# Kernel optimization log

Hardware: AMD Instinct MI355X
Metric: run time of the kernel (lower is better)

## Reference

```python
import jax, jax.numpy as jnp
import numpy as np
from jax.ops import segment_sum

N_NODES = 50000
N_EDGES = 800000
IN_DIM, HID_DIM, OUT_DIM = 128, 256, 128


def _glorot(key, shape):
    lim = np.sqrt(6.0 / (shape[0] + shape[1]))
    return jax.random.uniform(key, shape, jnp.float32, -lim, lim)


def setup_inputs() -> dict:
    key = jax.random.key(0)
    ks = jax.random.split(key, 4)
    x = jax.random.normal(ks[0], (N_NODES, IN_DIM), jnp.float32)
    edge_index = jax.random.randint(ks[1], (2, N_EDGES), 0, N_NODES, jnp.int64)
    W1 = _glorot(ks[2], (IN_DIM, HID_DIM))
    b1 = jnp.zeros((HID_DIM,), jnp.float32)
    W2 = _glorot(ks[3], (HID_DIM, OUT_DIM))
    b2 = jnp.zeros((OUT_DIM,), jnp.float32)
    return {"x": x, "edge_index": edge_index, "W1": W1, "b1": b1, "W2": W2, "b2": b2}


def gcn_conv(x, W, b, src, dst, n_nodes):
    # PyG GCNConv: x' = D^{-1/2} (A + I) D^{-1/2} (x W) + b
    h = x @ W  # [N, F_out]
    deg = segment_sum(jnp.ones_like(src, dtype=h.dtype), dst, num_segments=n_nodes) + 1.0  # +1 self loop
    dinv = jax.lax.rsqrt(deg)  # [N]
    norm = dinv[src] * dinv[dst]  # per-edge norm [E]
    msg = h[src] * norm[:, None]  # [E, F_out]
    agg = segment_sum(msg, dst, num_segments=n_nodes)
    agg = agg + h * (dinv * dinv)[:, None]  # self-loop term: norm_ii = dinv_i^2
    return agg + b


def reference(x, edge_index, W1, b1, W2, b2):
    src, dst = edge_index[0], edge_index[1]
    h = gcn_conv(x, W1, b1, src, dst, N_NODES)
    h = jax.nn.relu(h)
    out = gcn_conv(h, W2, b2, src, dst, N_NODES)
    return out
```

## Files before the change

kernel.cpp:

```cpp
#include <hip/hip_runtime.h>

#define N_NODES 50000
#define N_EDGES 800000
#define IN_DIM  128
#define HID_DIM 256
#define OUT_DIM 128
#define BUCKET_CAP 64
#define NCOARSE 391
#define BINSZ 128
#define CHUNK 4000
#define NBLK1 200
#define SEGCAP 32
#define HLD 264
#define GROWS 64

typedef __attribute__((ext_vector_type(8))) short short8;
typedef __attribute__((ext_vector_type(4))) float f32x4;

__device__ inline ushort f2b(float f) {
    union { float f; unsigned u; } v; v.f = f;
    return (ushort)((v.u + 0x7FFFu + ((v.u >> 16) & 1u)) >> 16);
}
__device__ inline float b2f(ushort h) {
    union { unsigned u; float f; } v; v.u = ((unsigned)h) << 16;
    return v.f;
}
__device__ inline float2 u2f2(unsigned u) {
    float2 r; r.x = b2f((ushort)(u & 0xFFFFu)); r.y = b2f((ushort)(u >> 16)); return r;
}
__device__ inline unsigned f2u2(float a, float b) {
    return (unsigned)f2b(a) | ((unsigned)f2b(b) << 16);
}
__device__ inline void fma8(float2* acc, uint4 u, float n) {
    float2 v0 = u2f2(u.x), v1 = u2f2(u.y), v2 = u2f2(u.z), v3 = u2f2(u.w);
    acc[0].x += v0.x * n; acc[0].y += v0.y * n;
    acc[1].x += v1.x * n; acc[1].y += v1.y * n;
    acc[2].x += v2.x * n; acc[2].y += v2.y * n;
    acc[3].x += v3.x * n; acc[3].y += v3.y * n;
}


__global__ __launch_bounds__(256) void prep_kernel(const float* __restrict__ x,
                                                   const float* __restrict__ W1,
                                                   const float* __restrict__ W2,
                                                   const int* __restrict__ src,
                                                   const int* __restrict__ dst,
                                                   ushort* __restrict__ xb,
                                                   ushort* __restrict__ w1t,
                                                   ushort* __restrict__ w2t,
                                                   int* __restrict__ bcnt,
                                                   int* __restrict__ binbuf) {
    __shared__ int vals[CHUNK];
    __shared__ ushort lpos[CHUNK];
    __shared__ ushort lbin[CHUNK];
    __shared__ int hist[NCOARSE];
    const int b = blockIdx.x;
    const int t = threadIdx.x;
    if (b < 6250) {
        int i = b * 256 + t;
        float4 v = ((const float4*)x)[i];
        ushort4 o; o.x = f2b(v.x); o.y = f2b(v.y); o.z = f2b(v.z); o.w = f2b(v.w);
        ((ushort4*)xb)[i] = o;
    } else if (b < 6506) {
        int i = (b - 6250) * 256 + t;
        if (i < 32768) {
            int n = i >> 7, k = i & 127;
            w1t[i] = f2b(W1[k * HID_DIM + n]);
        } else {
            int j = i - 32768;
            int n = j >> 8, k = j & 255;
            w2t[j] = f2b(W2[k * OUT_DIM + n]);
        }
    } else {
        const int blk = b - 6506;
        const int e0 = blk * CHUNK;
        for (int i = t; i < NCOARSE; i += 256) hist[i] = 0;
        __syncthreads();
        for (int i = t; i < CHUNK; i += 256) {
            int s = src[e0 + i], d = dst[e0 + i];
            int bin = d >> 7;
            vals[i] = (s << 7) | (d & 127);
            lbin[i] = (ushort)bin;
            lpos[i] = (ushort)atomicAdd(&hist[bin], 1);
        }
        __syncthreads();
        for (int i = t; i < NCOARSE; i += 256) {
            int h = hist[i]; if (h > SEGCAP) h = SEGCAP;
            bcnt[i * NBLK1 + blk] = h;
        }
        for (int i = t; i < CHUNK; i += 256) {
            int bin = lbin[i];
            int p = lpos[i];
            if (p < SEGCAP) binbuf[((size_t)bin * NBLK1 + blk) * SEGCAP + p] = vals[i];
        }
    }
}


__global__ __launch_bounds__(256) void binpass2_kernel(const int* __restrict__ bcnt,
                                                       const int* __restrict__ binbuf,
                                                       int* __restrict__ cnt,
                                                       float* __restrict__ dinv,
                                                       int* __restrict__ bucket) {
    __shared__ int lcnt[BINSZ];
    __shared__ int lm[NBLK1];
    __shared__ int lbuck[BINSZ * BUCKET_CAP];
    const int bin = blockIdx.x;
    const int t = threadIdx.x;
    if (t < BINSZ) lcnt[t] = 0;
    if (t < NBLK1) lm[t] = bcnt[bin * NBLK1 + t];
    __syncthreads();
    const int* bb = binbuf + (size_t)bin * NBLK1 * SEGCAP;
    for (int f = t; f < NBLK1 * SEGCAP; f += 256) {
        int blk = f >> 5;
        int sl = f & 31;
        if (sl < lm[blk]) {
            int v = bb[f];
            int dl = v & 127;
            int pos = atomicAdd(&lcnt[dl], 1);
            if (pos < BUCKET_CAP) lbuck[dl * BUCKET_CAP + pos] = v >> 7;
        }
    }
    __syncthreads();
    const int node0 = bin * BINSZ;
    int node = node0 + t;
    if (t < BINSZ && node < N_NODES) {
        int c = lcnt[t] > BUCKET_CAP ? BUCKET_CAP : lcnt[t];
        cnt[node] = c;
        dinv[node] = rsqrtf((float)c + 1.0f);
    }
    int nvalid = N_NODES - node0; if (nvalid > BINSZ) nvalid = BINSZ;
    if (nvalid <= 0) return;
    int total4 = (nvalid * BUCKET_CAP) >> 2;
    int4* d4 = (int4*)(bucket + (size_t)node0 * BUCKET_CAP);
    const int4* s4 = (const int4*)lbuck;
    for (int j = t; j < total4; j += 256) d4[j] = s4[j];
}


__global__ __launch_bounds__(256) void gather0_kernel(const int* __restrict__ cnt,
                                                      const int* __restrict__ bucket,
                                                      const float* __restrict__ dinv,
                                                      const ushort* __restrict__ xb,
                                                      ushort* __restrict__ aggxb) {
    const int w = blockIdx.x * 4 + (threadIdx.x >> 6);
    const int lane = threadIdx.x & 63;
    const int grp = lane >> 4, sub = lane & 15;
    const int n = cnt[w];
    const float dd = dinv[w];
    int sv = 0; float nv = 0.f;
    if (lane < n) { sv = bucket[w * BUCKET_CAP + lane]; nv = dinv[sv] * dd; }

    float2 acc[4];
    if (grp == 0) {
        uint4 su = ((const uint4*)(xb + (size_t)w * IN_DIM))[sub];
        float sd = dd * dd;
        acc[0] = u2f2(su.x); acc[1] = u2f2(su.y); acc[2] = u2f2(su.z); acc[3] = u2f2(su.w);
#pragma unroll
        for (int j = 0; j < 4; ++j) { acc[j].x *= sd; acc[j].y *= sd; }
    } else {
#pragma unroll
        for (int j = 0; j < 4; ++j) acc[j] = {0.f, 0.f};
    }

    const int nr = (n + 15) & ~15;
    for (int i = 0; i < nr; i += 16) {
        int s0 = __shfl(sv, i + grp),      s1 = __shfl(sv, i + 4 + grp);
        int s2 = __shfl(sv, i + 8 + grp),  s3 = __shfl(sv, i + 12 + grp);
        float n0 = __shfl(nv, i + grp),     n1 = __shfl(nv, i + 4 + grp);
        float n2 = __shfl(nv, i + 8 + grp), n3 = __shfl(nv, i + 12 + grp);
        uint4 u0 = ((const uint4*)(xb + (size_t)s0 * IN_DIM))[sub];
        uint4 u1 = ((const uint4*)(xb + (size_t)s1 * IN_DIM))[sub];
        uint4 u2 = ((const uint4*)(xb + (size_t)s2 * IN_DIM))[sub];
        uint4 u3 = ((const uint4*)(xb + (size_t)s3 * IN_DIM))[sub];
        fma8(acc, u0, n0); fma8(acc, u1, n1); fma8(acc, u2, n2); fma8(acc, u3, n3);
    }
#pragma unroll
    for (int j = 0; j < 4; ++j) {
        acc[j].x += __shfl_down(acc[j].x, 32); acc[j].y += __shfl_down(acc[j].y, 32);
        acc[j].x += __shfl_down(acc[j].x, 16); acc[j].y += __shfl_down(acc[j].y, 16);
    }
    if (lane < 16) {
        uint4 o = {f2u2(acc[0].x, acc[0].y), f2u2(acc[1].x, acc[1].y),
                   f2u2(acc[2].x, acc[2].y), f2u2(acc[3].x, acc[3].y)};
        ((uint4*)(aggxb + (size_t)w * IN_DIM))[sub] = o;
    }
}


__global__ __launch_bounds__(256, 2) void gemm12_mfma(const ushort* __restrict__ aggxb,
                                                      const ushort* __restrict__ w1t,
                                                      const float* __restrict__ b1,
                                                      const ushort* __restrict__ w2t,
                                                      ushort* __restrict__ h2b) {
    __shared__ ushort Hs[GROWS * HLD];
    const int row0 = blockIdx.x * GROWS;
    const int wv = threadIdx.x >> 6;
    const int lane = threadIdx.x & 63;
    const int l15 = lane & 15, q = lane >> 4;

    short8 bf1[16];
#pragma unroll
    for (int kb = 0; kb < 4; ++kb)
#pragma unroll
        for (int t = 0; t < 4; ++t) {
            int col = wv * 64 + t * 16 + l15;
            bf1[kb * 4 + t] = *(const short8*)(w1t + (size_t)col * IN_DIM + kb * 32 + q * 8);
        }
    short8 af[4][4];
#pragma unroll
    for (int sub = 0; sub < 4; ++sub) {
        int ar = row0 + sub * 16 + l15;
        if (ar >= N_NODES) ar = N_NODES - 1;
        const ushort* ab = aggxb + (size_t)ar * IN_DIM + q * 8;
#pragma unroll
        for (int kb = 0; kb < 4; ++kb) af[sub][kb] = *(const short8*)(ab + kb * 32);
    }
    f32x4 acc1[4][4] = {};
#pragma unroll
    for (int sub = 0; sub < 4; ++sub)
#pragma unroll
        for (int kb = 0; kb < 4; ++kb)
#pragma unroll
            for (int t = 0; t < 4; ++t)
                acc1[sub][t] = __builtin_amdgcn_mfma_f32_16x16x32_bf16(
                    af[sub][kb], bf1[kb * 4 + t], acc1[sub][t], 0, 0, 0);
#pragma unroll
    for (int t = 0; t < 4; ++t) {
        int col = wv * 64 + t * 16 + l15;
        float bias = b1[col];
#pragma unroll
        for (int sub = 0; sub < 4; ++sub)
#pragma unroll
            for (int r = 0; r < 4; ++r) {
                int row = sub * 16 + q * 4 + r;
                float v = acc1[sub][t][r] + bias;
                Hs[row * HLD + col] = f2b(v > 0.f ? v : 0.f);
            }
    }
    __syncthreads();

    short8 bf2[16];
#pragma unroll
    for (int kb = 0; kb < 8; ++kb)
#pragma unroll
        for (int t = 0; t < 2; ++t) {
            int col = wv * 32 + t * 16 + l15;
            bf2[kb * 2 + t] = *(const short8*)(w2t + (size_t)col * HID_DIM + kb * 32 + q * 8);
        }
    f32x4 acc2[4][2] = {};
#pragma unroll
    for (int sub = 0; sub < 4; ++sub) {
        const ushort* hb = Hs + (sub * 16 + l15) * HLD + q * 8;
#pragma unroll
        for (int kb = 0; kb < 8; ++kb) {
            short8 a = *(const short8*)(hb + kb * 32);
#pragma unroll
            for (int t = 0; t < 2; ++t)
                acc2[sub][t] = __builtin_amdgcn_mfma_f32_16x16x32_bf16(
                    a, bf2[kb * 2 + t], acc2[sub][t], 0, 0, 0);
        }
    }
#pragma unroll
    for (int sub = 0; sub < 4; ++sub)
#pragma unroll
        for (int t = 0; t < 2; ++t) {
            int col = wv * 32 + t * 16 + l15;
#pragma unroll
            for (int r = 0; r < 4; ++r) {
                int row = row0 + sub * 16 + q * 4 + r;
                if (row < N_NODES)
                    h2b[(size_t)row * OUT_DIM + col] = f2b(acc2[sub][t][r]);
            }
        }
}


__global__ __launch_bounds__(256) void gather2_kernel(const int* __restrict__ cnt,
                                                      const int* __restrict__ bucket,
                                                      const float* __restrict__ dinv,
                                                      const ushort* __restrict__ h2b,
                                                      const float* __restrict__ b2,
                                                      float* __restrict__ out) {
    const int w = blockIdx.x * 4 + (threadIdx.x >> 6);
    const int lane = threadIdx.x & 63;
    const int grp = lane >> 4, sub = lane & 15;
    const int n = cnt[w];
    const float dd = dinv[w];
    int sv = 0; float nv = 0.f;
    if (lane < n) { sv = bucket[w * BUCKET_CAP + lane]; nv = dinv[sv] * dd; }

    float2 acc[4];
    if (grp == 0) {
        uint4 su = ((const uint4*)(h2b + (size_t)w * OUT_DIM))[sub];
        float sd = dd * dd;
        acc[0] = u2f2(su.x); acc[1] = u2f2(su.y); acc[2] = u2f2(su.z); acc[3] = u2f2(su.w);
#pragma unroll
        for (int j = 0; j < 4; ++j) { acc[j].x *= sd; acc[j].y *= sd; }
    } else {
#pragma unroll
        for (int j = 0; j < 4; ++j) acc[j] = {0.f, 0.f};
    }

    const int nr = (n + 15) & ~15;
    for (int i = 0; i < nr; i += 16) {
        int s0 = __shfl(sv, i + grp),      s1 = __shfl(sv, i + 4 + grp);
        int s2 = __shfl(sv, i + 8 + grp),  s3 = __shfl(sv, i + 12 + grp);
        float n0 = __shfl(nv, i + grp),     n1 = __shfl(nv, i + 4 + grp);
        float n2 = __shfl(nv, i + 8 + grp), n3 = __shfl(nv, i + 12 + grp);
        uint4 u0 = ((const uint4*)(h2b + (size_t)s0 * OUT_DIM))[sub];
        uint4 u1 = ((const uint4*)(h2b + (size_t)s1 * OUT_DIM))[sub];
        uint4 u2 = ((const uint4*)(h2b + (size_t)s2 * OUT_DIM))[sub];
        uint4 u3 = ((const uint4*)(h2b + (size_t)s3 * OUT_DIM))[sub];
        fma8(acc, u0, n0); fma8(acc, u1, n1); fma8(acc, u2, n2); fma8(acc, u3, n3);
    }
#pragma unroll
    for (int j = 0; j < 4; ++j) {
        acc[j].x += __shfl_down(acc[j].x, 32); acc[j].y += __shfl_down(acc[j].y, 32);
        acc[j].x += __shfl_down(acc[j].x, 16); acc[j].y += __shfl_down(acc[j].y, 16);
    }
    if (lane < 16) {
        const float4* bp = (const float4*)b2;
        float4 b0 = bp[sub * 2], b1v = bp[sub * 2 + 1];
        float4 o0 = {acc[0].x + b0.x, acc[0].y + b0.y, acc[1].x + b0.z, acc[1].y + b0.w};
        float4 o1 = {acc[2].x + b1v.x, acc[2].y + b1v.y, acc[3].x + b1v.z, acc[3].y + b1v.w};
        float4* op = (float4*)(out + (size_t)w * OUT_DIM);
        op[sub * 2] = o0;
        op[sub * 2 + 1] = o1;
    }
}

extern "C" void kernel_launch(void* const* d_in, const int* in_sizes, int n_in,
                              void* d_out, int out_size, void* d_ws, size_t ws_size,
                              hipStream_t stream) {
    const float* x  = (const float*)d_in[0];
    const int*   ei = (const int*)d_in[1];
    const float* W1 = (const float*)d_in[2];
    const float* b1 = (const float*)d_in[3];
    const float* W2 = (const float*)d_in[4];
    const float* b2 = (const float*)d_in[5];
    float* out = (float*)d_out;

    const int* src = ei;
    const int* dst = ei + N_EDGES;

    char* ws = (char*)d_ws;
    int*    bcnt   = (int*)(ws);
    int*    cnt    = (int*)(ws + 320000);
    float*  dinv   = (float*)(ws + 520000);
    int*    bucket = (int*)(ws + 720000);
    int*    binbuf = (int*)(ws + 13520000);
    ushort* xb     = (ushort*)(ws + 23532800);
    ushort* w1t    = (ushort*)(ws + 36332800);
    ushort* w2t    = (ushort*)(ws + 36398336);
    ushort* aggxb  = (ushort*)(ws + 36463872);
    ushort* h2b    = (ushort*)(ws + 49263872);

    prep_kernel<<<6706, 256, 0, stream>>>(x, W1, W2, src, dst, xb, w1t, w2t, bcnt, binbuf);
    binpass2_kernel<<<NCOARSE, 256, 0, stream>>>(bcnt, binbuf, cnt, dinv, bucket);

    gather0_kernel<<<N_NODES / 4, 256, 0, stream>>>(cnt, bucket, dinv, xb, aggxb);
    gemm12_mfma<<<(N_NODES + GROWS - 1) / GROWS, 256, 0, stream>>>(aggxb, w1t, b1, w2t, h2b);

    gather2_kernel<<<N_NODES / 4, 256, 0, stream>>>(cnt, bucket, dinv, h2b, b2, out);
}
```

Measured before the change: 206.4 us.

## Split gather feature tables into four column-quarter planes for cache locality

Stores the bf16 node features and the layer-2 projected features as four separate 32-column planes instead of row-major 128-column rows. Each gather block now handles one quarter of the columns for four nodes, and the block index is swizzled so that concurrently running blocks share the same plane. The intent is a smaller working set per plane (3.2 MB) that fits better in L2/MALL during the random neighbour gathers. In exchange there are four times as many blocks, each gather row read is only 64 bytes, the index and norm loads repeat four times, and the cross-lane reduction gets longer.

New measurement: 300.6 us. +45.6%, slower.

```diff
diff --git a/kernel.cpp b/kernel.cpp
--- a/kernel.cpp
+++ b/kernel.cpp
@@ -13,6 +13,7 @@
 #define SEGCAP 32
 #define HLD 264
 #define GROWS 64
+#define QS 1600000
 
 typedef __attribute__((ext_vector_type(8))) short short8;
 typedef __attribute__((ext_vector_type(4))) float f32x4;
@@ -45,7 +46,7 @@
                                                    const float* __restrict__ W2,
                                                    const int* __restrict__ src,
                                                    const int* __restrict__ dst,
-                                                   ushort* __restrict__ xb,
+                                                   ushort* __restrict__ xq,
                                                    ushort* __restrict__ w1t,
                                                    ushort* __restrict__ w2t,
                                                    int* __restrict__ bcnt,
@@ -60,7 +61,9 @@
         int i = b * 256 + t;
         float4 v = ((const float4*)x)[i];
         ushort4 o; o.x = f2b(v.x); o.y = f2b(v.y); o.z = f2b(v.z); o.w = f2b(v.w);
-        ((ushort4*)xb)[i] = o;
+        int node = i >> 5, r = i & 31;
+        int q = r >> 3, wi = r & 7;
+        ((ushort4*)xq)[(size_t)q * (N_NODES * 8) + node * 8 + wi] = o;
     } else if (b < 6506) {
         int i = (b - 6250) * 256 + t;
         if (i < 32768) {
@@ -141,49 +144,46 @@
 __global__ __launch_bounds__(256) void gather0_kernel(const int* __restrict__ cnt,
                                                       const int* __restrict__ bucket,
                                                       const float* __restrict__ dinv,
-                                                      const ushort* __restrict__ xb,
+                                                      const ushort* __restrict__ xq,
                                                       ushort* __restrict__ aggxb) {
-    const int w = blockIdx.x * 4 + (threadIdx.x >> 6);
+    const int bid = blockIdx.x;
+    const int q = (bid & 7) >> 1;
+    const int i = ((bid >> 3) << 1) | (bid & 1);
+    const int w = i * 4 + (threadIdx.x >> 6);
     const int lane = threadIdx.x & 63;
-    const int grp = lane >> 4, sub = lane & 15;
+    const ushort* __restrict__ xqq = xq + (size_t)q * QS;
     const int n = cnt[w];
     const float dd = dinv[w];
     int sv = 0; float nv = 0.f;
     if (lane < n) { sv = bucket[w * BUCKET_CAP + lane]; nv = dinv[sv] * dd; }
 
-    float2 acc[4];
-    if (grp == 0) {
-        uint4 su = ((const uint4*)(xb + (size_t)w * IN_DIM))[sub];
+    float2 acc[4] = {};
+    const int nr = (n + 15) & ~15;
+    for (int it = 0; it < nr; it += 16) {
+        int es = it + (lane >> 2);
+        int s = __shfl(sv, es);
+        float f = __shfl(nv, es);
+        uint4 u = *(const uint4*)(xqq + (size_t)s * 32 + (lane & 3) * 8);
+        fma8(acc, u, f);
+    }
+#pragma unroll
+    for (int st = 32; st >= 4; st >>= 1)
+#pragma unroll
+        for (int j = 0; j < 4; ++j) {
+            acc[j].x += __shfl_down(acc[j].x, st);
+            acc[j].y += __shfl_down(acc[j].y, st);
+        }
+    if (lane < 4) {
+        uint4 su = *(const uint4*)(xqq + (size_t)w * 32 + lane * 8);
         float sd = dd * dd;
-        acc[0] = u2f2(su.x); acc[1] = u2f2(su.y); acc[2] = u2f2(su.z); acc[3] = u2f2(su.w);
-#pragma unroll
-        for (int j = 0; j < 4; ++j) { acc[j].x *= sd; acc[j].y *= sd; }
-    } else {
-#pragma unroll
-        for (int j = 0; j < 4; ++j) acc[j] = {0.f, 0.f};
-    }
-
-    const int nr = (n + 15) & ~15;
-    for (int i = 0; i < nr; i += 16) {
-        int s0 = __shfl(sv, i + grp),      s1 = __shfl(sv, i + 4 + grp);
-        int s2 = __shfl(sv, i + 8 + grp),  s3 = __shfl(sv, i + 12 + grp);
-        float n0 = __shfl(nv, i + grp),     n1 = __shfl(nv, i + 4 + grp);
-        float n2 = __shfl(nv, i + 8 + grp), n3 = __shfl(nv, i + 12 + grp);
-        uint4 u0 = ((const uint4*)(xb + (size_t)s0 * IN_DIM))[sub];
-        uint4 u1 = ((const uint4*)(xb + (size_t)s1 * IN_DIM))[sub];
-        uint4 u2 = ((const uint4*)(xb + (size_t)s2 * IN_DIM))[sub];
-        uint4 u3 = ((const uint4*)(xb + (size_t)s3 * IN_DIM))[sub];
-        fma8(acc, u0, n0); fma8(acc, u1, n1); fma8(acc, u2, n2); fma8(acc, u3, n3);
-    }
-#pragma unroll
-    for (int j = 0; j < 4; ++j) {
-        acc[j].x += __shfl_down(acc[j].x, 32); acc[j].y += __shfl_down(acc[j].y, 32);
-        acc[j].x += __shfl_down(acc[j].x, 16); acc[j].y += __shfl_down(acc[j].y, 16);
-    }
-    if (lane < 16) {
+        float2 s0 = u2f2(su.x), s1 = u2f2(su.y), s2 = u2f2(su.z), s3 = u2f2(su.w);
+        acc[0].x += s0.x * sd; acc[0].y += s0.y * sd;
+        acc[1].x += s1.x * sd; acc[1].y += s1.y * sd;
+        acc[2].x += s2.x * sd; acc[2].y += s2.y * sd;
+        acc[3].x += s3.x * sd; acc[3].y += s3.y * sd;
         uint4 o = {f2u2(acc[0].x, acc[0].y), f2u2(acc[1].x, acc[1].y),
                    f2u2(acc[2].x, acc[2].y), f2u2(acc[3].x, acc[3].y)};
-        ((uint4*)(aggxb + (size_t)w * IN_DIM))[sub] = o;
+        *(uint4*)(aggxb + (size_t)w * IN_DIM + q * 32 + lane * 8) = o;
     }
 }
 
@@ -192,7 +192,7 @@
                                                       const ushort* __restrict__ w1t,
                                                       const float* __restrict__ b1,
                                                       const ushort* __restrict__ w2t,
-                                                      ushort* __restrict__ h2b) {
+                                                      ushort* __restrict__ h2q) {
     __shared__ ushort Hs[GROWS * HLD];
     const int row0 = blockIdx.x * GROWS;
     const int wv = threadIdx.x >> 6;
@@ -265,12 +265,12 @@
     for (int sub = 0; sub < 4; ++sub)
 #pragma unroll
         for (int t = 0; t < 2; ++t) {
-            int col = wv * 32 + t * 16 + l15;
+            int cq = t * 16 + l15;
 #pragma unroll
             for (int r = 0; r < 4; ++r) {
                 int row = row0 + sub * 16 + q * 4 + r;
                 if (row < N_NODES)
-                    h2b[(size_t)row * OUT_DIM + col] = f2b(acc2[sub][t][r]);
+                    h2q[(size_t)wv * QS + (size_t)row * 32 + cq] = f2b(acc2[sub][t][r]);
             }
         }
 }
@@ -279,54 +279,51 @@
 __global__ __launch_bounds__(256) void gather2_kernel(const int* __restrict__ cnt,
                                                       const int* __restrict__ bucket,
                                                       const float* __restrict__ dinv,
-                                                      const ushort* __restrict__ h2b,
+                                                      const ushort* __restrict__ h2q,
                                                       const float* __restrict__ b2,
                                                       float* __restrict__ out) {
-    const int w = blockIdx.x * 4 + (threadIdx.x >> 6);
+    const int bid = blockIdx.x;
+    const int q = (bid & 7) >> 1;
+    const int i = ((bid >> 3) << 1) | (bid & 1);
+    const int w = i * 4 + (threadIdx.x >> 6);
     const int lane = threadIdx.x & 63;
-    const int grp = lane >> 4, sub = lane & 15;
+    const ushort* __restrict__ hqq = h2q + (size_t)q * QS;
     const int n = cnt[w];
     const float dd = dinv[w];
     int sv = 0; float nv = 0.f;
     if (lane < n) { sv = bucket[w * BUCKET_CAP + lane]; nv = dinv[sv] * dd; }
 
-    float2 acc[4];
-    if (grp == 0) {
-        uint4 su = ((const uint4*)(h2b + (size_t)w * OUT_DIM))[sub];
+    float2 acc[4] = {};
+    const int nr = (n + 15) & ~15;
+    for (int it = 0; it < nr; it += 16) {
+        int es = it + (lane >> 2);
+        int s = __shfl(sv, es);
+        float f = __shfl(nv, es);
+        uint4 u = *(const uint4*)(hqq + (size_t)s * 32 + (lane & 3) * 8);
+        fma8(acc, u, f);
+    }
+#pragma unroll
+    for (int st = 32; st >= 4; st >>= 1)
+#pragma unroll
+        for (int j = 0; j < 4; ++j) {
+            acc[j].x += __shfl_down(acc[j].x, st);
+            acc[j].y += __shfl_down(acc[j].y, st);
+        }
+    if (lane < 4) {
+        uint4 su = *(const uint4*)(hqq + (size_t)w * 32 + lane * 8);
         float sd = dd * dd;
-        acc[0] = u2f2(su.x); acc[1] = u2f2(su.y); acc[2] = u2f2(su.z); acc[3] = u2f2(su.w);
-#pragma unroll
-        for (int j = 0; j < 4; ++j) { acc[j].x *= sd; acc[j].y *= sd; }
-    } else {
-#pragma unroll
-        for (int j = 0; j < 4; ++j) acc[j] = {0.f, 0.f};
-    }
-
-    const int nr = (n + 15) & ~15;
-    for (int i = 0; i < nr; i += 16) {
-        int s0 = __shfl(sv, i + grp),      s1 = __shfl(sv, i + 4 + grp);
-        int s2 = __shfl(sv, i + 8 + grp),  s3 = __shfl(sv, i + 12 + grp);
-        float n0 = __shfl(nv, i + grp),     n1 = __shfl(nv, i + 4 + grp);
-        float n2 = __shfl(nv, i + 8 + grp), n3 = __shfl(nv, i + 12 + grp);
-        uint4 u0 = ((const uint4*)(h2b + (size_t)s0 * OUT_DIM))[sub];
-        uint4 u1 = ((const uint4*)(h2b + (size_t)s1 * OUT_DIM))[sub];
-        uint4 u2 = ((const uint4*)(h2b + (size_t)s2 * OUT_DIM))[sub];
-        uint4 u3 = ((const uint4*)(h2b + (size_t)s3 * OUT_DIM))[sub];
-        fma8(acc, u0, n0); fma8(acc, u1, n1); fma8(acc, u2, n2); fma8(acc, u3, n3);
-    }
-#pragma unroll
-    for (int j = 0; j < 4; ++j) {
-        acc[j].x += __shfl_down(acc[j].x, 32); acc[j].y += __shfl_down(acc[j].y, 32);
-        acc[j].x += __shfl_down(acc[j].x, 16); acc[j].y += __shfl_down(acc[j].y, 16);
-    }
-    if (lane < 16) {
+        float2 s0 = u2f2(su.x), s1 = u2f2(su.y), s2 = u2f2(su.z), s3 = u2f2(su.w);
+        acc[0].x += s0.x * sd; acc[0].y += s0.y * sd;
+        acc[1].x += s1.x * sd; acc[1].y += s1.y * sd;
+        acc[2].x += s2.x * sd; acc[2].y += s2.y * sd;
+        acc[3].x += s3.x * sd; acc[3].y += s3.y * sd;
         const float4* bp = (const float4*)b2;
-        float4 b0 = bp[sub * 2], b1v = bp[sub * 2 + 1];
-        float4 o0 = {acc[0].x + b0.x, acc[0].y + b0.y, acc[1].x + b0.z, acc[1].y + b0.w};
-        float4 o1 = {acc[2].x + b1v.x, acc[2].y + b1v.y, acc[3].x + b1v.z, acc[3].y + b1v.w};
-        float4* op = (float4*)(out + (size_t)w * OUT_DIM);
-        op[sub * 2] = o0;
-        op[sub * 2 + 1] = o1;
+        float4 ba = bp[q * 8 + lane * 2], bb = bp[q * 8 + lane * 2 + 1];
+        float4 o0 = {acc[0].x + ba.x, acc[0].y + ba.y, acc[1].x + ba.z, acc[1].y + ba.w};
+        float4 o1 = {acc[2].x + bb.x, acc[2].y + bb.y, acc[3].x + bb.z, acc[3].y + bb.w};
+        float4* op = (float4*)(out + (size_t)w * OUT_DIM + q * 32);
+        op[lane * 2] = o0;
+        op[lane * 2 + 1] = o1;
     }
 }
 
@@ -350,17 +347,17 @@
     float*  dinv   = (float*)(ws + 520000);
     int*    bucket = (int*)(ws + 720000);
     int*    binbuf = (int*)(ws + 13520000);
-    ushort* xb     = (ushort*)(ws + 23532800);
+    ushort* xq     = (ushort*)(ws + 23532800);
     ushort* w1t    = (ushort*)(ws + 36332800);
     ushort* w2t    = (ushort*)(ws + 36398336);
     ushort* aggxb  = (ushort*)(ws + 36463872);
-    ushort* h2b    = (ushort*)(ws + 49263872);
-
-    prep_kernel<<<6706, 256, 0, stream>>>(x, W1, W2, src, dst, xb, w1t, w2t, bcnt, binbuf);
+    ushort* h2q    = (ushort*)(ws + 49263872);
+
+    prep_kernel<<<6706, 256, 0, stream>>>(x, W1, W2, src, dst, xq, w1t, w2t, bcnt, binbuf);
     binpass2_kernel<<<NCOARSE, 256, 0, stream>>>(bcnt, binbuf, cnt, dinv, bucket);
 
-    gather0_kernel<<<N_NODES / 4, 256, 0, stream>>>(cnt, bucket, dinv, xb, aggxb);
-    gemm12_mfma<<<(N_NODES + GROWS - 1) / GROWS, 256, 0, stream>>>(aggxb, w1t, b1, w2t, h2b);
-
-    gather2_kernel<<<N_NODES / 4, 256, 0, stream>>>(cnt, bucket, dinv, h2b, b2, out);
-}
+    gather0_kernel<<<50000, 256, 0, stream>>>(cnt, bucket, dinv, xq, aggxb);
+    gemm12_mfma<<<(N_NODES + GROWS - 1) / GROWS, 256, 0, stream>>>(aggxb, w1t, b1, w2t, h2q);
+
+    gather2_kernel<<<50000, 256, 0, stream>>>(cnt, bucket, dinv, h2q, b2, out);
+}
```

## Store neighbor buckets as 16-bit indices and sort each bucket by source range

Applied to the files above, without the earlier changes.

Neighbor buckets shrink from int32 to ushort source indices (all nodes are below 65536), which halves bucket write and read traffic. Within binpass2, each node's bucket also gets a counting sort into seven coarse source ranges (index >> 13) before being written out, so the gather kernels visit source rows in a more clustered order for better cache locality. The sort is a serial per-thread loop over up to 64 entries in shared memory and needs a second shared buffer. The workspace offsets are repacked to match the smaller bucket array.

After: 207.7 us. About the same (+0.6%).

```diff
diff --git a/kernel.cpp b/kernel.cpp
--- a/kernel.cpp
+++ b/kernel.cpp
@@ -101,10 +101,11 @@
                                                        const int* __restrict__ binbuf,
                                                        int* __restrict__ cnt,
                                                        float* __restrict__ dinv,
-                                                       int* __restrict__ bucket) {
+                                                       ushort* __restrict__ bucket) {
     __shared__ int lcnt[BINSZ];
     __shared__ int lm[NBLK1];
-    __shared__ int lbuck[BINSZ * BUCKET_CAP];
+    __shared__ ushort lbuck[BINSZ * BUCKET_CAP];
+    __shared__ ushort lbuck2[BINSZ * BUCKET_CAP];
     const int bin = blockIdx.x;
     const int t = threadIdx.x;
     if (t < BINSZ) lcnt[t] = 0;
@@ -118,28 +119,47 @@
             int v = bb[f];
             int dl = v & 127;
             int pos = atomicAdd(&lcnt[dl], 1);
-            if (pos < BUCKET_CAP) lbuck[dl * BUCKET_CAP + pos] = v >> 7;
+            if (pos < BUCKET_CAP) lbuck[dl * BUCKET_CAP + pos] = (ushort)(v >> 7);
         }
     }
     __syncthreads();
     const int node0 = bin * BINSZ;
-    int node = node0 + t;
-    if (t < BINSZ && node < N_NODES) {
-        int c = lcnt[t] > BUCKET_CAP ? BUCKET_CAP : lcnt[t];
-        cnt[node] = c;
-        dinv[node] = rsqrtf((float)c + 1.0f);
-    }
+    if (t < BINSZ) {
+        int c = lcnt[t]; if (c > BUCKET_CAP) c = BUCKET_CAP;
+        const ushort* in = lbuck + t * BUCKET_CAP;
+        ushort* o = lbuck2 + t * BUCKET_CAP;
+        unsigned long long hh = 0ULL;
+        for (int i = 0; i < c; ++i) hh += 1ULL << ((in[i] >> 13) * 9);
+        unsigned long long oo = 0ULL; int run = 0;
+#pragma unroll
+        for (int k = 0; k < 7; ++k) {
+            oo |= (unsigned long long)run << (k * 9);
+            run += (int)((hh >> (k * 9)) & 511ULL);
+        }
+        for (int i = 0; i < c; ++i) {
+            int k = in[i] >> 13;
+            int pos = (int)((oo >> (k * 9)) & 511ULL);
+            oo += 1ULL << (k * 9);
+            o[pos] = in[i];
+        }
+        int node = node0 + t;
+        if (node < N_NODES) {
+            cnt[node] = c;
+            dinv[node] = rsqrtf((float)c + 1.0f);
+        }
+    }
+    __syncthreads();
     int nvalid = N_NODES - node0; if (nvalid > BINSZ) nvalid = BINSZ;
     if (nvalid <= 0) return;
-    int total4 = (nvalid * BUCKET_CAP) >> 2;
-    int4* d4 = (int4*)(bucket + (size_t)node0 * BUCKET_CAP);
-    const int4* s4 = (const int4*)lbuck;
-    for (int j = t; j < total4; j += 256) d4[j] = s4[j];
+    int total8 = (nvalid * BUCKET_CAP) >> 3;
+    uint4* d4 = (uint4*)(bucket + (size_t)node0 * BUCKET_CAP);
+    const uint4* s4 = (const uint4*)lbuck2;
+    for (int j = t; j < total8; j += 256) d4[j] = s4[j];
 }
 
 
 __global__ __launch_bounds__(256) void gather0_kernel(const int* __restrict__ cnt,
-                                                      const int* __restrict__ bucket,
+                                                      const ushort* __restrict__ bucket,
                                                       const float* __restrict__ dinv,
                                                       const ushort* __restrict__ xb,
                                                       ushort* __restrict__ aggxb) {
@@ -149,7 +169,7 @@
     const int n = cnt[w];
     const float dd = dinv[w];
     int sv = 0; float nv = 0.f;
-    if (lane < n) { sv = bucket[w * BUCKET_CAP + lane]; nv = dinv[sv] * dd; }
+    if (lane < n) { sv = (int)bucket[w * BUCKET_CAP + lane]; nv = dinv[sv] * dd; }
 
     float2 acc[4];
     if (grp == 0) {
@@ -277,7 +297,7 @@
 
 
 __global__ __launch_bounds__(256) void gather2_kernel(const int* __restrict__ cnt,
-                                                      const int* __restrict__ bucket,
+                                                      const ushort* __restrict__ bucket,
                                                       const float* __restrict__ dinv,
                                                       const ushort* __restrict__ h2b,
                                                       const float* __restrict__ b2,
@@ -288,7 +308,7 @@
     const int n = cnt[w];
     const float dd = dinv[w];
     int sv = 0; float nv = 0.f;
-    if (lane < n) { sv = bucket[w * BUCKET_CAP + lane]; nv = dinv[sv] * dd; }
+    if (lane < n) { sv = (int)bucket[w * BUCKET_CAP + lane]; nv = dinv[sv] * dd; }
 
     float2 acc[4];
     if (grp == 0) {
@@ -348,13 +368,13 @@
     int*    bcnt   = (int*)(ws);
     int*    cnt    = (int*)(ws + 320000);
     float*  dinv   = (float*)(ws + 520000);
-    int*    bucket = (int*)(ws + 720000);
-    int*    binbuf = (int*)(ws + 13520000);
-    ushort* xb     = (ushort*)(ws + 23532800);
-    ushort* w1t    = (ushort*)(ws + 36332800);
-    ushort* w2t    = (ushort*)(ws + 36398336);
-    ushort* aggxb  = (ushort*)(ws + 36463872);
-    ushort* h2b    = (ushort*)(ws + 49263872);
+    ushort* bucket = (ushort*)(ws + 720000);
+    int*    binbuf = (int*)(ws + 7120000);
+    ushort* xb     = (ushort*)(ws + 17132800);
+    ushort* w1t    = (ushort*)(ws + 29932800);
+    ushort* w2t    = (ushort*)(ws + 29998336);
+    ushort* aggxb  = (ushort*)(ws + 30063872);
+    ushort* h2b    = (ushort*)(ws + 42863872);
 
     prep_kernel<<<6706, 256, 0, stream>>>(x, W1, W2, src, dst, xb, w1t, w2t, bcnt, binbuf);
     binpass2_kernel<<<NCOARSE, 256, 0, stream>>>(bcnt, binbuf, cnt, dinv, bucket);
```

## Precompute edge norms, compact bucket to ushort, split gathers into column quarters

Applied to the files above, without the earlier changes.

Degree counting moves into the prep kernel as global atomics, followed by a separate dinv kernel. The bin pass now writes 16-bit source ids and a precomputed per-edge norm buffer. Both gather kernels split each row into four 32-column quarters across four times as many blocks, with each lane loading 4 bytes per edge instead of 16. This removes the dependent dinv[src] lookups from the gathers and adds parallelism. The cost is many more small, less-coalesced random loads, an extra launch plus memset, global atomics, and the norm buffer traffic. dinv now uses the uncapped degree while the buckets stay capped.

Result: slower. 364.4 us (+76.6%).

```diff
diff --git a/kernel.cpp b/kernel.cpp
--- a/kernel.cpp
+++ b/kernel.cpp
@@ -13,6 +13,7 @@
 #define SEGCAP 32
 #define HLD 264
 #define GROWS 64
+#define NQBLK 12500
 
 typedef __attribute__((ext_vector_type(8))) short short8;
 typedef __attribute__((ext_vector_type(4))) float f32x4;
@@ -30,13 +31,6 @@
 }
 __device__ inline unsigned f2u2(float a, float b) {
     return (unsigned)f2b(a) | ((unsigned)f2b(b) << 16);
-}
-__device__ inline void fma8(float2* acc, uint4 u, float n) {
-    float2 v0 = u2f2(u.x), v1 = u2f2(u.y), v2 = u2f2(u.z), v3 = u2f2(u.w);
-    acc[0].x += v0.x * n; acc[0].y += v0.y * n;
-    acc[1].x += v1.x * n; acc[1].y += v1.y * n;
-    acc[2].x += v2.x * n; acc[2].y += v2.y * n;
-    acc[3].x += v3.x * n; acc[3].y += v3.y * n;
 }
 
 
@@ -48,6 +42,7 @@
                                                    ushort* __restrict__ xb,
                                                    ushort* __restrict__ w1t,
                                                    ushort* __restrict__ w2t,
+                                                   int* __restrict__ cnt,
                                                    int* __restrict__ bcnt,
                                                    int* __restrict__ binbuf) {
     __shared__ int vals[CHUNK];
@@ -78,6 +73,7 @@
         __syncthreads();
         for (int i = t; i < CHUNK; i += 256) {
             int s = src[e0 + i], d = dst[e0 + i];
+            atomicAdd(&cnt[d], 1);
             int bin = d >> 7;
             vals[i] = (s << 7) | (d & 127);
             lbin[i] = (ushort)bin;
@@ -97,17 +93,30 @@
 }
 
 
+__global__ __launch_bounds__(256) void dinv_kernel(const int* __restrict__ cnt,
+                                                   float* __restrict__ dinv) {
+    int i = blockIdx.x * 256 + threadIdx.x;
+    if (i < N_NODES) dinv[i] = rsqrtf((float)cnt[i] + 1.0f);
+}
+
+
 __global__ __launch_bounds__(256) void binpass2_kernel(const int* __restrict__ bcnt,
                                                        const int* __restrict__ binbuf,
-                                                       int* __restrict__ cnt,
-                                                       float* __restrict__ dinv,
-                                                       int* __restrict__ bucket) {
+                                                       const float* __restrict__ dinv,
+                                                       ushort* __restrict__ bucket,
+                                                       float* __restrict__ normbuf) {
     __shared__ int lcnt[BINSZ];
     __shared__ int lm[NBLK1];
-    __shared__ int lbuck[BINSZ * BUCKET_CAP];
+    __shared__ float ldv[BINSZ];
+    __shared__ ushort lbuck[BINSZ * BUCKET_CAP];
     const int bin = blockIdx.x;
     const int t = threadIdx.x;
-    if (t < BINSZ) lcnt[t] = 0;
+    const int node0 = bin * BINSZ;
+    if (t < BINSZ) {
+        lcnt[t] = 0;
+        int nd = node0 + t;
+        ldv[t] = nd < N_NODES ? dinv[nd] : 0.f;
+    }
     if (t < NBLK1) lm[t] = bcnt[bin * NBLK1 + t];
     __syncthreads();
     const int* bb = binbuf + (size_t)bin * NBLK1 * SEGCAP;
@@ -118,72 +127,57 @@
             int v = bb[f];
             int dl = v & 127;
             int pos = atomicAdd(&lcnt[dl], 1);
-            if (pos < BUCKET_CAP) lbuck[dl * BUCKET_CAP + pos] = v >> 7;
+            if (pos < BUCKET_CAP) lbuck[dl * BUCKET_CAP + pos] = (ushort)(v >> 7);
         }
     }
     __syncthreads();
-    const int node0 = bin * BINSZ;
-    int node = node0 + t;
-    if (t < BINSZ && node < N_NODES) {
-        int c = lcnt[t] > BUCKET_CAP ? BUCKET_CAP : lcnt[t];
-        cnt[node] = c;
-        dinv[node] = rsqrtf((float)c + 1.0f);
-    }
-    int nvalid = N_NODES - node0; if (nvalid > BINSZ) nvalid = BINSZ;
-    if (nvalid <= 0) return;
-    int total4 = (nvalid * BUCKET_CAP) >> 2;
-    int4* d4 = (int4*)(bucket + (size_t)node0 * BUCKET_CAP);
-    const int4* s4 = (const int4*)lbuck;
-    for (int j = t; j < total4; j += 256) d4[j] = s4[j];
+    for (int idx = t; idx < BINSZ * BUCKET_CAP; idx += 256) {
+        int node = idx >> 6, sl = idx & 63;
+        int nd = node0 + node;
+        if (nd >= N_NODES) break;
+        int c = lcnt[node]; if (c > BUCKET_CAP) c = BUCKET_CAP;
+        bool val = sl < c;
+        ushort s = val ? lbuck[idx] : (ushort)0;
+        float nm = val ? dinv[s] * ldv[node] : 0.f;
+        size_t g = (size_t)nd * BUCKET_CAP + sl;
+        bucket[g] = s;
+        normbuf[g] = nm;
+    }
 }
 
 
 __global__ __launch_bounds__(256) void gather0_kernel(const int* __restrict__ cnt,
-                                                      const int* __restrict__ bucket,
+                                                      const ushort* __restrict__ bucket,
+                                                      const float* __restrict__ normbuf,
                                                       const float* __restrict__ dinv,
                                                       const ushort* __restrict__ xb,
                                                       ushort* __restrict__ aggxb) {
-    const int w = blockIdx.x * 4 + (threadIdx.x >> 6);
+    const int bid = blockIdx.x;
+    const int q = bid / NQBLK;
+    const int w = (bid % NQBLK) * 4 + (threadIdx.x >> 6);
     const int lane = threadIdx.x & 63;
-    const int grp = lane >> 4, sub = lane & 15;
-    const int n = cnt[w];
-    const float dd = dinv[w];
-    int sv = 0; float nv = 0.f;
-    if (lane < n) { sv = bucket[w * BUCKET_CAP + lane]; nv = dinv[sv] * dd; }
-
-    float2 acc[4];
-    if (grp == 0) {
-        uint4 su = ((const uint4*)(xb + (size_t)w * IN_DIM))[sub];
-        float sd = dd * dd;
-        acc[0] = u2f2(su.x); acc[1] = u2f2(su.y); acc[2] = u2f2(su.z); acc[3] = u2f2(su.w);
-#pragma unroll
-        for (int j = 0; j < 4; ++j) { acc[j].x *= sd; acc[j].y *= sd; }
-    } else {
-#pragma unroll
-        for (int j = 0; j < 4; ++j) acc[j] = {0.f, 0.f};
-    }
-
-    const int nr = (n + 15) & ~15;
-    for (int i = 0; i < nr; i += 16) {
-        int s0 = __shfl(sv, i + grp),      s1 = __shfl(sv, i + 4 + grp);
-        int s2 = __shfl(sv, i + 8 + grp),  s3 = __shfl(sv, i + 12 + grp);
-        float n0 = __shfl(nv, i + grp),     n1 = __shfl(nv, i + 4 + grp);
-        float n2 = __shfl(nv, i + 8 + grp), n3 = __shfl(nv, i + 12 + grp);
-        uint4 u0 = ((const uint4*)(xb + (size_t)s0 * IN_DIM))[sub];
-        uint4 u1 = ((const uint4*)(xb + (size_t)s1 * IN_DIM))[sub];
-        uint4 u2 = ((const uint4*)(xb + (size_t)s2 * IN_DIM))[sub];
-        uint4 u3 = ((const uint4*)(xb + (size_t)s3 * IN_DIM))[sub];
-        fma8(acc, u0, n0); fma8(acc, u1, n1); fma8(acc, u2, n2); fma8(acc, u3, n3);
-    }
-#pragma unroll
-    for (int j = 0; j < 4; ++j) {
-        acc[j].x += __shfl_down(acc[j].x, 32); acc[j].y += __shfl_down(acc[j].y, 32);
-        acc[j].x += __shfl_down(acc[j].x, 16); acc[j].y += __shfl_down(acc[j].y, 16);
-    }
+    const int e = lane >> 4;
+    const int c = lane & 15;
+    int ctv = cnt[w];
+    int n = ctv > BUCKET_CAP ? BUCKET_CAP : ctv;
+    int sv = (int)bucket[(size_t)w * BUCKET_CAP + lane];
+    float nv = normbuf[(size_t)w * BUCKET_CAP + lane];
+    const ushort* xs = xb + q * 32 + c * 2;
+    float2 acc = {0.f, 0.f};
+    const int nr = (n + 3) & ~3;
+    for (int it = 0; it < nr; it += 4) {
+        int s = __shfl(sv, it + e);
+        float f = __shfl(nv, it + e);
+        float2 v = u2f2(*(const unsigned*)(xs + (size_t)s * IN_DIM));
+        acc.x += v.x * f; acc.y += v.y * f;
+    }
+    acc.x += __shfl_down(acc.x, 32); acc.y += __shfl_down(acc.y, 32);
+    acc.x += __shfl_down(acc.x, 16); acc.y += __shfl_down(acc.y, 16);
     if (lane < 16) {
-        uint4 o = {f2u2(acc[0].x, acc[0].y), f2u2(acc[1].x, acc[1].y),
-                   f2u2(acc[2].x, acc[2].y), f2u2(acc[3].x, acc[3].y)};
-        ((uint4*)(aggxb + (size_t)w * IN_DIM))[sub] = o;
+        float dd = dinv[w], sd = dd * dd;
+        float2 sx = u2f2(*(const unsigned*)(xs + (size_t)w * IN_DIM));
+        acc.x += sx.x * sd; acc.y += sx.y * sd;
+        *(unsigned*)(aggxb + (size_t)w * IN_DIM + q * 32 + lane * 2) = f2u2(acc.x, acc.y);
     }
 }
 
@@ -277,56 +271,40 @@
 
 
 __global__ __launch_bounds__(256) void gather2_kernel(const int* __restrict__ cnt,
-                                                      const int* __restrict__ bucket,
+                                                      const ushort* __restrict__ bucket,
+                                                      const float* __restrict__ normbuf,
                                                       const float* __restrict__ dinv,
                                                       const ushort* __restrict__ h2b,
                                                       const float* __restrict__ b2,
                                                       float* __restrict__ out) {
-    const int w = blockIdx.x * 4 + (threadIdx.x >> 6);
+    const int bid = blockIdx.x;
+    const int q = bid / NQBLK;
+    const int w = (bid % NQBLK) * 4 + (threadIdx.x >> 6);
     const int lane = threadIdx.x & 63;
-    const int grp = lane >> 4, sub = lane & 15;
-    const int n = cnt[w];
-    const float dd = dinv[w];
-    int sv = 0; float nv = 0.f;
-    if (lane < n) { sv = bucket[w * BUCKET_CAP + lane]; nv = dinv[sv] * dd; }
-
-    float2 acc[4];
-    if (grp == 0) {
-        uint4 su = ((const uint4*)(h2b + (size_t)w * OUT_DIM))[sub];
-        float sd = dd * dd;
-        acc[0] = u2f2(su.x); acc[1] = u2f2(su.y); acc[2] = u2f2(su.z); acc[3] = u2f2(su.w);
-#pragma unroll
-        for (int j = 0; j < 4; ++j) { acc[j].x *= sd; acc[j].y *= sd; }
-    } else {
-#pragma unroll
-        for (int j = 0; j < 4; ++j) acc[j] = {0.f, 0.f};
-    }
-
-    const int nr = (n + 15) & ~15;
-    for (int i = 0; i < nr; i += 16) {
-        int s0 = __shfl(sv, i + grp),      s1 = __shfl(sv, i + 4 + grp);
-        int s2 = __shfl(sv, i + 8 + grp),  s3 = __shfl(sv, i + 12 + grp);
-        float n0 = __shfl(nv, i + grp),     n1 = __shfl(nv, i + 4 + grp);
-        float n2 = __shfl(nv, i + 8 + grp), n3 = __shfl(nv, i + 12 + grp);
-        uint4 u0 = ((const uint4*)(h2b + (size_t)s0 * OUT_DIM))[sub];
-        uint4 u1 = ((const uint4*)(h2b + (size_t)s1 * OUT_DIM))[sub];
-        uint4 u2 = ((const uint4*)(h2b + (size_t)s2 * OUT_DIM))[sub];
-        uint4 u3 = ((const uint4*)(h2b + (size_t)s3 * OUT_DIM))[sub];
-        fma8(acc, u0, n0); fma8(acc, u1, n1); fma8(acc, u2, n2); fma8(acc, u3, n3);
-    }
-#pragma unroll
-    for (int j = 0; j < 4; ++j) {
-        acc[j].x += __shfl_down(acc[j].x, 32); acc[j].y += __shfl_down(acc[j].y, 32);
-        acc[j].x += __shfl_down(acc[j].x, 16); acc[j].y += __shfl_down(acc[j].y, 16);
-    }
+    const int e = lane >> 4;
+    const int c = lane & 15;
+    int ctv = cnt[w];
+    int n = ctv > BUCKET_CAP ? BUCKET_CAP : ctv;
+    int sv = (int)bucket[(size_t)w * BUCKET_CAP + lane];
+    float nv = normbuf[(size_t)w * BUCKET_CAP + lane];
+    const ushort* hs = h2b + q * 32 + c * 2;
+    float2 acc = {0.f, 0.f};
+    const int nr = (n + 3) & ~3;
+    for (int it = 0; it < nr; it += 4) {
+        int s = __shfl(sv, it + e);
+        float f = __shfl(nv, it + e);
+        float2 v = u2f2(*(const unsigned*)(hs + (size_t)s * OUT_DIM));
+        acc.x += v.x * f; acc.y += v.y * f;
+    }
+    acc.x += __shfl_down(acc.x, 32); acc.y += __shfl_down(acc.y, 32);
+    acc.x += __shfl_down(acc.x, 16); acc.y += __shfl_down(acc.y, 16);
     if (lane < 16) {
-        const float4* bp = (const float4*)b2;
-        float4 b0 = bp[sub * 2], b1v = bp[sub * 2 + 1];
-        float4 o0 = {acc[0].x + b0.x, acc[0].y + b0.y, acc[1].x + b0.z, acc[1].y + b0.w};
-        float4 o1 = {acc[2].x + b1v.x, acc[2].y + b1v.y, acc[3].x + b1v.z, acc[3].y + b1v.w};
-        float4* op = (float4*)(out + (size_t)w * OUT_DIM);
-        op[sub * 2] = o0;
-        op[sub * 2 + 1] = o1;
+        float dd = dinv[w], sd = dd * dd;
+        float2 sx = u2f2(*(const unsigned*)(hs + (size_t)w * OUT_DIM));
+        float2 bb = *(const float2*)(b2 + q * 32 + lane * 2);
+        acc.x += sx.x * sd + bb.x;
+        acc.y += sx.y * sd + bb.y;
+        *(float2*)(out + (size_t)w * OUT_DIM + q * 32 + lane * 2) = acc;
     }
 }
 
@@ -345,22 +323,27 @@
     const int* dst = ei + N_EDGES;
 
     char* ws = (char*)d_ws;
-    int*    bcnt   = (int*)(ws);
-    int*    cnt    = (int*)(ws + 320000);
-    float*  dinv   = (float*)(ws + 520000);
-    int*    bucket = (int*)(ws + 720000);
-    int*    binbuf = (int*)(ws + 13520000);
-    ushort* xb     = (ushort*)(ws + 23532800);
-    ushort* w1t    = (ushort*)(ws + 36332800);
-    ushort* w2t    = (ushort*)(ws + 36398336);
-    ushort* aggxb  = (ushort*)(ws + 36463872);
-    ushort* h2b    = (ushort*)(ws + 49263872);
-
-    prep_kernel<<<6706, 256, 0, stream>>>(x, W1, W2, src, dst, xb, w1t, w2t, bcnt, binbuf);
-    binpass2_kernel<<<NCOARSE, 256, 0, stream>>>(bcnt, binbuf, cnt, dinv, bucket);
-
-    gather0_kernel<<<N_NODES / 4, 256, 0, stream>>>(cnt, bucket, dinv, xb, aggxb);
+    int*    bcnt    = (int*)(ws);
+    int*    cnt     = (int*)(ws + 320000);
+    float*  dinv    = (float*)(ws + 520000);
+    ushort* bucket  = (ushort*)(ws + 720000);
+    float*  normbuf = (float*)(ws + 7120000);
+    int*    binbuf  = (int*)(ws + 19920000);
+    ushort* xb      = (ushort*)(ws + 29932800);
+    ushort* w1t     = (ushort*)(ws + 42732800);
+    ushort* w2t     = (ushort*)(ws + 42798336);
+    ushort* aggxb   = (ushort*)(ws + 42863872);
+    ushort* h2b     = (ushort*)(ws + 55663872);
+
+    hipMemsetAsync(cnt, 0, N_NODES * sizeof(int), stream);
+
+    prep_kernel<<<6706, 256, 0, stream>>>(x, W1, W2, src, dst, xb, w1t, w2t,
+                                          cnt, bcnt, binbuf);
+    dinv_kernel<<<196, 256, 0, stream>>>(cnt, dinv);
+    binpass2_kernel<<<NCOARSE, 256, 0, stream>>>(bcnt, binbuf, dinv, bucket, normbuf);
+
+    gather0_kernel<<<4 * NQBLK, 256, 0, stream>>>(cnt, bucket, normbuf, dinv, xb, aggxb);
     gemm12_mfma<<<(N_NODES + GROWS - 1) / GROWS, 256, 0, stream>>>(aggxb, w1t, b1, w2t, h2b);
 
-    gather2_kernel<<<N_NODES / 4, 256, 0, stream>>>(cnt, bucket, dinv, h2b, b2, out);
-}
+    gather2_kernel<<<4 * NQBLK, 256, 0, stream>>>(cnt, bucket, normbuf, dinv, h2b, b2, out);
+}
```
